# Kernel tuning notes

Measured on AMD Instinct MI355X. Metric: run time of the kernel, lower is better.

Reference implementation:

```python
import jax, jax.numpy as jnp
import numpy as np

N_NODES = 100000
N_EDGES = 1600000
IN_CH = 128
OUT_CH = 64
HID = 2 * OUT_CH  # 128


def _gcn_conv(x, src, dst, deg_inv_sqrt, W, b, n_nodes):
    """PyG GCNConv with symmetric normalization; self-loops already in (src, dst)."""
    h = x @ W                                   # [N, F_out] dense GEMM
    norm = deg_inv_sqrt[src] * deg_inv_sqrt[dst]  # [E+N]
    msg = h[src] * norm[:, None]                # gather + scale (irregular)
    out = jax.ops.segment_sum(msg, dst, num_segments=n_nodes)  # scatter-add
    return out + b


def setup_inputs() -> dict:
    key = jax.random.key(0)
    ks = jax.random.split(key, 8)
    x = jax.random.normal(ks[0], (N_NODES, IN_CH), dtype=jnp.float32)
    edge_index = jax.random.randint(ks[1], (2, N_EDGES), 0, N_NODES, dtype=jnp.int64)
    # Glorot-ish params for the three GCNConv layers
    W1 = jax.random.normal(ks[2], (IN_CH, HID), dtype=jnp.float32) / np.sqrt(IN_CH)
    b1 = jnp.zeros((HID,), dtype=jnp.float32)
    W_mu = jax.random.normal(ks[3], (HID, OUT_CH), dtype=jnp.float32) / np.sqrt(HID)
    b_mu = jnp.zeros((OUT_CH,), dtype=jnp.float32)
    W_ls = jax.random.normal(ks[4], (HID, OUT_CH), dtype=jnp.float32) / np.sqrt(HID)
    b_ls = jnp.zeros((OUT_CH,), dtype=jnp.float32)
    return {"x": x, "edge_index": edge_index, "W1": W1, "b1": b1,
            "W_mu": W_mu, "b_mu": b_mu, "W_ls": W_ls, "b_ls": b_ls}


def reference(x, edge_index, W1, b1, W_mu, b_mu, W_ls, b_ls):
    n = x.shape[0]
    # GCNConv adds self-loops to the same edge_index in every layer; do it once.
    loop = jnp.arange(n, dtype=edge_index.dtype)
    src = jnp.concatenate([edge_index[0], loop])  # source / row
    dst = jnp.concatenate([edge_index[1], loop])  # target / col
    # Symmetric normalization: deg over targets with unit edge weights.
    deg = jax.ops.segment_sum(jnp.ones_like(dst, dtype=x.dtype), dst, num_segments=n)
    deg_inv_sqrt = jnp.where(deg > 0, jax.lax.rsqrt(jnp.maximum(deg, 1.0)), 0.0)

    h = jax.nn.relu(_gcn_conv(x, src, dst, deg_inv_sqrt, W1, b1, n))
    mu = _gcn_conv(h, src, dst, deg_inv_sqrt, W_mu, b_mu, n)
    logstd = _gcn_conv(h, src, dst, deg_inv_sqrt, W_ls, b_ls, n)
    return mu, logstd
```

## Files before the change

### kernel.cpp

```cpp
#include <hip/hip_runtime.h>
#include <hip/hip_bf16.h>
#include <stdint.h>


static inline size_t align_up(size_t x, size_t a) { return (x + a - 1) / a * a; }

typedef __attribute__((ext_vector_type(8))) short short8;
typedef __attribute__((ext_vector_type(4))) float f32x4;

#define BSHIFT 7
#define BNODES 128
#define CHUNKS 512
#define NBMAX 1024

__device__ inline unsigned short f2bf(float f) {
    unsigned u = __float_as_uint(f);
    unsigned r = (u + 0x7FFFu + ((u >> 16) & 1u)) >> 16;
    return (unsigned short)r;
}
__device__ inline float bf2f(unsigned v16) {
    return __uint_as_float(v16 << 16);
}


__global__ void detect_i64_kernel(const int* __restrict__ ei, int nwords_check, int* __restrict__ flag) {
    __shared__ int any_nz;
    if (threadIdx.x == 0) any_nz = 0;
    __syncthreads();
    int nz = 0;
    for (int i = threadIdx.x; i < nwords_check; i += blockDim.x) {
        if (ei[2 * i + 1] != 0) nz = 1;
    }
    if (nz) atomicOr(&any_nz, 1);
    __syncthreads();
    if (threadIdx.x == 0) flag[0] = any_nz ? 0 : 1;
}

__device__ inline int load_idx(const void* ei, const int* flag, size_t pos, int n) {
    int v;
    if (flag[0]) v = (int)((const long long*)ei)[pos];
    else         v = ((const int*)ei)[pos];
    return (v < 0) ? 0 : (v >= n ? n - 1 : v);
}


__global__ __launch_bounds__(256) void chunk_hist_kernel(
        const void* __restrict__ ei, const int* __restrict__ flag,
        int* __restrict__ hmat, int E, int n, int nb, int epc) {
    __shared__ int hist[NBMAX];
    const int c = blockIdx.x, t = threadIdx.x;
    for (int i = t; i < nb; i += 256) hist[i] = 0;
    __syncthreads();
    const int lo = c * epc, hi = min(E, lo + epc);
    for (int i = lo + t; i < hi; i += 256) {
        int d = load_idx(ei, flag, (size_t)E + i, n);
        atomicAdd(&hist[d >> BSHIFT], 1);
    }
    __syncthreads();
    for (int i = t; i < nb; i += 256) hmat[(size_t)c * nb + i] = hist[i];
}


__global__ __launch_bounds__(256) void bucket_scan_cols_kernel(
        int* __restrict__ hmat, int* __restrict__ btot, int nb) {
    __shared__ int tmp[256];
    const int b = blockIdx.x, t = threadIdx.x;
    const int c0 = 2 * t;
    int va = hmat[(size_t)c0 * nb + b];
    int vb = hmat[(size_t)(c0 + 1) * nb + b];
    int pair = va + vb;
    tmp[t] = pair;
    __syncthreads();
    for (int off = 1; off < 256; off <<= 1) {
        int u = (t >= off) ? tmp[t - off] : 0;
        __syncthreads();
        tmp[t] += u;
        __syncthreads();
    }
    int excl = tmp[t] - pair;
    hmat[(size_t)c0 * nb + b] = excl;
    hmat[(size_t)(c0 + 1) * nb + b] = excl + va;
    if (t == 255) btot[b] = tmp[255];
}


__global__ void base_scan_kernel(const int* __restrict__ btot, int* __restrict__ bbase, int nb) {
    __shared__ int tmp[NBMAX];
    int t = threadIdx.x;
    int v = (t < nb) ? btot[t] : 0;
    tmp[t] = v;
    __syncthreads();
    for (int off = 1; off < NBMAX; off <<= 1) {
        int u = (t >= off) ? tmp[t - off] : 0;
        __syncthreads();
        tmp[t] += u;
        __syncthreads();
    }
    if (t < nb) bbase[t] = tmp[t] - v;
}


__global__ __launch_bounds__(256) void chunk_scatter_kernel(
        const void* __restrict__ ei, const int* __restrict__ flag,
        const int* __restrict__ hmat, const int* __restrict__ bbase,
        unsigned* __restrict__ binned, int E, int n, int nb, int epc) {
    __shared__ int lcur[NBMAX];
    const int c = blockIdx.x, t = threadIdx.x;
    for (int i = t; i < nb; i += 256) lcur[i] = hmat[(size_t)c * nb + i] + bbase[i];
    __syncthreads();
    const int lo = c * epc, hi = min(E, lo + epc);
    for (int i = lo + t; i < hi; i += 256) {
        int s = load_idx(ei, flag, i, n);
        int d = load_idx(ei, flag, (size_t)E + i, n);
        int b = d >> BSHIFT;
        int pos = atomicAdd(&lcur[b], 1);
        binned[pos] = ((unsigned)s << BSHIFT) | (unsigned)(d & (BNODES - 1));
    }
}


__global__ __launch_bounds__(256) void bucket_csr_kernel(
        const unsigned* __restrict__ binned, const int* __restrict__ bbase,
        const int* __restrict__ btot, float* __restrict__ dis,
        int* __restrict__ row_beg, int* __restrict__ row_end,
        int* __restrict__ csr_src, int n) {
    __shared__ int ldeg[BNODES];
    __shared__ int lscan[BNODES];
    __shared__ int lcur[BNODES];
    const int b = blockIdx.x;
    const int t = threadIdx.x;
    const int base = bbase[b];
    const int cnt = btot[b];

    if (t < BNODES) ldeg[t] = 0;
    __syncthreads();
    for (int i = t; i < cnt; i += 256) {
        unsigned w = binned[base + i];
        atomicAdd(&ldeg[w & (BNODES - 1)], 1);
    }
    __syncthreads();
    int v = (t < BNODES) ? ldeg[t] : 0;
    if (t < BNODES) lscan[t] = v;
    __syncthreads();
    for (int off = 1; off < BNODES; off <<= 1) {
        int u = (t < BNODES && t >= off) ? lscan[t - off] : 0;
        __syncthreads();
        if (t < BNODES) lscan[t] += u;
        __syncthreads();
    }
    if (t < BNODES) {
        int excl = lscan[t] - v;
        lcur[t] = excl;
        int node = (b << BSHIFT) + t;
        if (node < n) {
            dis[node] = rsqrtf((float)v + 1.0f);
            row_beg[node] = base + excl;
            row_end[node] = base + excl + v;
        }
    }
    __syncthreads();
    for (int i = t; i < cnt; i += 256) {
        unsigned w = binned[base + i];
        int pos = atomicAdd(&lcur[w & (BNODES - 1)], 1);
        csr_src[base + pos] = (int)(w >> BSHIFT);
    }
}


__global__ void prep_weights_kernel(const float* __restrict__ W1,
                                    const float* __restrict__ Wmu,
                                    const float* __restrict__ Wls,
                                    unsigned short* __restrict__ Wt1,
                                    unsigned short* __restrict__ Wtcat) {
    int idx = blockIdx.x * 256 + threadIdx.x;
    if (idx < 16384) {
        int c = idx >> 7, k = idx & 127;
        Wt1[c * 128 + k] = f2bf(W1[k * 128 + c]);
    } else if (idx < 32768) {
        int i = idx - 16384;
        int j = i >> 7, k = i & 127;
        float v = (j < 64) ? Wmu[k * 64 + j] : Wls[k * 64 + (j - 64)];
        Wtcat[j * 128 + k] = f2bf(v);
    }
}


template <int MODE>
__global__ __launch_bounds__(256) void mfma_gemm_kernel(
        const void* __restrict__ Ax, const unsigned short* __restrict__ Wt,
        const float* __restrict__ biasA, const float* __restrict__ biasB,
        void* __restrict__ outA, void* __restrict__ outB, int n) {
    __shared__ unsigned short ws[128 * 136];
    const int tid = threadIdx.x;
    const int wave = tid >> 6, lane = tid & 63;
    const int brow = blockIdx.x * 64 + wave * 16;
    const int lr = lane & 15;
    const int kg = lane >> 4;
    const int k0 = kg * 8;

    for (int i = tid; i < 2048; i += 256) {
        int r = i >> 4, ci = i & 15;
        *(short8*)&ws[r * 136 + ci * 8] = *(const short8*)&Wt[r * 128 + ci * 8];
    }
    __syncthreads();

    int arow = brow + lr;
    if (arow >= n) arow = n - 1;

    f32x4 acc[8];
#pragma unroll
    for (int t = 0; t < 8; ++t) acc[t] = (f32x4){0.f, 0.f, 0.f, 0.f};

#pragma unroll
    for (int c = 0; c < 4; ++c) {
        short8 a;
        if (MODE == 0) {
            const float* ap = (const float*)Ax + (size_t)arow * 128 + c * 32 + k0;
            float4 lo = *(const float4*)ap;
            float4 hi = *(const float4*)(ap + 4);
            a[0] = (short)f2bf(lo.x); a[1] = (short)f2bf(lo.y);
            a[2] = (short)f2bf(lo.z); a[3] = (short)f2bf(lo.w);
            a[4] = (short)f2bf(hi.x); a[5] = (short)f2bf(hi.y);
            a[6] = (short)f2bf(hi.z); a[7] = (short)f2bf(hi.w);
        } else {
            a = *(const short8*)((const unsigned short*)Ax + (size_t)arow * 128 + c * 32 + k0);
        }
#pragma unroll
        for (int t = 0; t < 8; ++t) {
            short8 bfr = *(const short8*)&ws[(t * 16 + lr) * 136 + c * 32 + k0];
            acc[t] = __builtin_amdgcn_mfma_f32_16x16x32_bf16(a, bfr, acc[t], 0, 0, 0);
        }
    }

    if (MODE == 0) {
        unsigned short* out = (unsigned short*)outA;
#pragma unroll
        for (int t = 0; t < 8; ++t) {
            int col = t * 16 + lr;
#pragma unroll
            for (int r = 0; r < 4; ++r) {
                int row = brow + kg * 4 + r;
                if (row < n) out[(size_t)row * 128 + col] = f2bf(acc[t][r]);
            }
        }
    } else {
        float* oA = (float*)outA;
        float* oB = (float*)outB;
#pragma unroll
        for (int t = 0; t < 8; ++t) {
            int col = t * 16 + lr;
            float bv = (col < 64) ? biasA[col] : biasB[col - 64];
#pragma unroll
            for (int r = 0; r < 4; ++r) {
                int row = brow + kg * 4 + r;
                if (row < n) {
                    float v = acc[t][r] + bv;
                    if (col < 64) oA[(size_t)row * 64 + col] = v;
                    else          oB[(size_t)row * 64 + (col - 64)] = v;
                }
            }
        }
    }
}


__global__ __launch_bounds__(256) void csr_agg_kernel(
        const unsigned short* __restrict__ hin, const int* __restrict__ row_beg,
        const int* __restrict__ row_end, const int* __restrict__ csr_src,
        const float* __restrict__ dis, const float* __restrict__ bias,
        unsigned short* __restrict__ out, int n, int relu) {
    int node = blockIdx.x * 4 + (threadIdx.x >> 6);
    if (node >= n) return;
    const int lane = threadIdx.x & 63;
    const int hi_half = lane >> 5;
    const unsigned foff = (lane & 31) * 8;
    int beg = row_beg[node], end = row_end[node];
    float dv = dis[node];

    const char* hinb = (const char*)hin;

    float a0x = 0.f, a0y = 0.f, a0z = 0.f, a0w = 0.f;
    float a1x = 0.f, a1y = 0.f, a1z = 0.f, a1w = 0.f;
    float a2x = 0.f, a2y = 0.f, a2z = 0.f, a2w = 0.f;
    float a3x = 0.f, a3y = 0.f, a3z = 0.f, a3w = 0.f;

    int e = beg;
    for (; e + 7 < end; e += 8) {
        int s0 = csr_src[e + 0 + hi_half];
        int s1 = csr_src[e + 2 + hi_half];
        int s2 = csr_src[e + 4 + hi_half];
        int s3 = csr_src[e + 6 + hi_half];
        float w0 = dis[s0], w1 = dis[s1], w2 = dis[s2], w3 = dis[s3];
        uint2 d0 = *(const uint2*)(hinb + (size_t)s0 * 256 + foff);
        uint2 d1 = *(const uint2*)(hinb + (size_t)s1 * 256 + foff);
        uint2 d2 = *(const uint2*)(hinb + (size_t)s2 * 256 + foff);
        uint2 d3 = *(const uint2*)(hinb + (size_t)s3 * 256 + foff);
        a0x += bf2f(d0.x & 0xffffu) * w0; a0y += bf2f(d0.x >> 16) * w0;
        a0z += bf2f(d0.y & 0xffffu) * w0; a0w += bf2f(d0.y >> 16) * w0;
        a1x += bf2f(d1.x & 0xffffu) * w1; a1y += bf2f(d1.x >> 16) * w1;
        a1z += bf2f(d1.y & 0xffffu) * w1; a1w += bf2f(d1.y >> 16) * w1;
        a2x += bf2f(d2.x & 0xffffu) * w2; a2y += bf2f(d2.x >> 16) * w2;
        a2z += bf2f(d2.y & 0xffffu) * w2; a2w += bf2f(d2.y >> 16) * w2;
        a3x += bf2f(d3.x & 0xffffu) * w3; a3y += bf2f(d3.x >> 16) * w3;
        a3z += bf2f(d3.y & 0xffffu) * w3; a3w += bf2f(d3.y >> 16) * w3;
    }
    for (; e + 1 < end; e += 2) {
        int s = csr_src[e + hi_half];
        float w = dis[s];
        uint2 d = *(const uint2*)(hinb + (size_t)s * 256 + foff);
        a0x += bf2f(d.x & 0xffffu) * w; a0y += bf2f(d.x >> 16) * w;
        a0z += bf2f(d.y & 0xffffu) * w; a0w += bf2f(d.y >> 16) * w;
    }
    if (e < end) {
        int s = csr_src[e];
        float w = 0.5f * dis[s];
        uint2 d = *(const uint2*)(hinb + (size_t)s * 256 + foff);
        a1x += bf2f(d.x & 0xffffu) * w; a1y += bf2f(d.x >> 16) * w;
        a1z += bf2f(d.y & 0xffffu) * w; a1w += bf2f(d.y >> 16) * w;
    }

    float sx = (a0x + a1x) + (a2x + a3x);
    float sy = (a0y + a1y) + (a2y + a3y);
    float sz = (a0z + a1z) + (a2z + a3z);
    float sw = (a0w + a1w) + (a2w + a3w);
    sx += __shfl_xor(sx, 32, 64);
    sy += __shfl_xor(sy, 32, 64);
    sz += __shfl_xor(sz, 32, 64);
    sw += __shfl_xor(sw, 32, 64);

    uint2 sd = *(const uint2*)(hinb + (size_t)node * 256 + foff);
    sx = dv * (sx + dv * bf2f(sd.x & 0xffffu));
    sy = dv * (sy + dv * bf2f(sd.x >> 16));
    sz = dv * (sz + dv * bf2f(sd.y & 0xffffu));
    sw = dv * (sw + dv * bf2f(sd.y >> 16));

    if (bias) {
        float4 bb = *(const float4*)&bias[(lane & 31) * 4];
        sx += bb.x; sy += bb.y; sz += bb.z; sw += bb.w;
    }
    if (relu) {
        sx = fmaxf(sx, 0.f); sy = fmaxf(sy, 0.f);
        sz = fmaxf(sz, 0.f); sw = fmaxf(sw, 0.f);
    }
    if (lane < 32) {
        uint2 o;
        o.x = (unsigned)f2bf(sx) | ((unsigned)f2bf(sy) << 16);
        o.y = (unsigned)f2bf(sz) | ((unsigned)f2bf(sw) << 16);
        *(uint2*)((char*)out + (size_t)node * 256 + foff) = o;
    }
}


extern "C" void kernel_launch(void* const* d_in, const int* in_sizes, int n_in,
                              void* d_out, int out_size, void* d_ws, size_t ws_size,
                              hipStream_t stream) {
    const float* x   = (const float*)d_in[0];
    const void*  ei  = d_in[1];
    const float* W1  = (const float*)d_in[2];
    const float* b1  = (const float*)d_in[3];
    const float* Wmu = (const float*)d_in[4];
    const float* bmu = (const float*)d_in[5];
    const float* Wls = (const float*)d_in[6];
    const float* bls = (const float*)d_in[7];

    const int n = in_sizes[0] / 128;
    const int E = in_sizes[1] / 2;
    const int nb = (n + BNODES - 1) >> BSHIFT;
    const int epc = (E + CHUNKS - 1) / CHUNKS;

    float* out   = (float*)d_out;
    float* outMu = out;
    float* outLs = out + (size_t)n * 64;

    char* w = (char*)d_ws;
    auto alloc = [&](size_t bytes) { char* p = w; w += align_up(bytes, 256); return p; };
    int*            flag    = (int*)           alloc(256);
    int*            hmat    = (int*)           alloc((size_t)CHUNKS * nb * 4);
    int*            btot    = (int*)           alloc(NBMAX * 4);
    int*            bbase   = (int*)           alloc(NBMAX * 4);
    unsigned*       binned  = (unsigned*)      alloc((size_t)E * 4);
    int*            row_beg = (int*)           alloc((size_t)n * 4);
    int*            row_end = (int*)           alloc((size_t)n * 4);
    float*          dis     = (float*)         alloc((size_t)n * 4);
    int*            csr_src = (int*)           alloc((size_t)E * 4);
    unsigned short* Wt1     = (unsigned short*)alloc(128 * 128 * 2);
    unsigned short* Wtcat   = (unsigned short*)alloc(128 * 128 * 2);
    unsigned short* xW      = (unsigned short*)alloc((size_t)n * 128 * 2);
    unsigned short* h       = (unsigned short*)alloc((size_t)n * 128 * 2);
    unsigned short* hagg    = (unsigned short*)alloc((size_t)n * 128 * 2);

    detect_i64_kernel<<<1, 256, 0, stream>>>((const int*)ei, 1024, flag);
    chunk_hist_kernel<<<CHUNKS, 256, 0, stream>>>(ei, flag, hmat, E, n, nb, epc);
    bucket_scan_cols_kernel<<<nb, 256, 0, stream>>>(hmat, btot, nb);
    base_scan_kernel<<<1, NBMAX, 0, stream>>>(btot, bbase, nb);
    chunk_scatter_kernel<<<CHUNKS, 256, 0, stream>>>(ei, flag, hmat, bbase, binned, E, n, nb, epc);
    bucket_csr_kernel<<<nb, 256, 0, stream>>>(binned, bbase, btot, dis, row_beg, row_end,
                                              csr_src, n);
    prep_weights_kernel<<<128, 256, 0, stream>>>(W1, Wmu, Wls, Wt1, Wtcat);

    const int gblocks = (n + 63) / 64;

    mfma_gemm_kernel<0><<<gblocks, 256, 0, stream>>>(x, Wt1, nullptr, nullptr, xW, nullptr, n);
    csr_agg_kernel<<<(n + 3) / 4, 256, 0, stream>>>(xW, row_beg, row_end, csr_src,
                                                    dis, b1, h, n, 1);

    csr_agg_kernel<<<(n + 3) / 4, 256, 0, stream>>>(h, row_beg, row_end, csr_src,
                                                    dis, nullptr, hagg, n, 0);
    mfma_gemm_kernel<1><<<gblocks, 256, 0, stream>>>(hagg, Wtcat, bmu, bls, outMu, outLs, n);
}
```

Baseline: 239.5 us.

## Fuse second aggregation with output GEMM and inline int64 index detection

Merges the layer-2 CSR aggregation and the mu/logstd GEMM into one kernel. Each 1024-thread block aggregates 16 nodes into shared memory and then runs MFMA against the concatenated weights, which removes the hagg round trip through global memory. It also drops the separate int64-detection kernel by having each chunk block probe its own range. The trade-off is that every 16-node block reloads the full 128x128 weight tile into LDS, and half the waves sit idle during the GEMM phase.

```diff
diff --git a/kernel.cpp b/kernel.cpp
--- a/kernel.cpp
+++ b/kernel.cpp
@@ -22,38 +22,40 @@
     return __uint_as_float(v16 << 16);
 }
 
-
-__global__ void detect_i64_kernel(const int* __restrict__ ei, int nwords_check, int* __restrict__ flag) {
-    __shared__ int any_nz;
-    if (threadIdx.x == 0) any_nz = 0;
+__device__ inline bool detect_i64_local(const void* ei, int lo, int hi, int t) {
+    __shared__ int s_nz;
+    if (t == 0) s_nz = 0;
     __syncthreads();
     int nz = 0;
-    for (int i = threadIdx.x; i < nwords_check; i += blockDim.x) {
-        if (ei[2 * i + 1] != 0) nz = 1;
-    }
-    if (nz) atomicOr(&any_nz, 1);
-    __syncthreads();
-    if (threadIdx.x == 0) flag[0] = any_nz ? 0 : 1;
-}
-
-__device__ inline int load_idx(const void* ei, const int* flag, size_t pos, int n) {
+    int lim = min(hi, lo + 1024);
+    const int* p = (const int*)ei;
+    for (int i = lo + t; i < lim; i += 256) {
+        if (p[2 * i + 1] != 0) nz = 1;
+    }
+    if (nz) atomicOr(&s_nz, 1);
+    __syncthreads();
+    return s_nz == 0;
+}
+
+__device__ inline int load_idx2(const void* ei, bool is64, size_t pos, int n) {
     int v;
-    if (flag[0]) v = (int)((const long long*)ei)[pos];
-    else         v = ((const int*)ei)[pos];
+    if (is64) v = (int)((const long long*)ei)[pos];
+    else      v = ((const int*)ei)[pos];
     return (v < 0) ? 0 : (v >= n ? n - 1 : v);
 }
 
 
 __global__ __launch_bounds__(256) void chunk_hist_kernel(
-        const void* __restrict__ ei, const int* __restrict__ flag,
-        int* __restrict__ hmat, int E, int n, int nb, int epc) {
+        const void* __restrict__ ei, int* __restrict__ hmat,
+        int E, int n, int nb, int epc) {
     __shared__ int hist[NBMAX];
     const int c = blockIdx.x, t = threadIdx.x;
+    const int lo = min(E, c * epc), hi = min(E, lo + epc);
+    bool is64 = detect_i64_local(ei, lo, hi, t);
     for (int i = t; i < nb; i += 256) hist[i] = 0;
     __syncthreads();
-    const int lo = c * epc, hi = min(E, lo + epc);
     for (int i = lo + t; i < hi; i += 256) {
-        int d = load_idx(ei, flag, (size_t)E + i, n);
+        int d = load_idx2(ei, is64, (size_t)E + i, n);
         atomicAdd(&hist[d >> BSHIFT], 1);
     }
     __syncthreads();
@@ -101,17 +103,18 @@
 
 
 __global__ __launch_bounds__(256) void chunk_scatter_kernel(
-        const void* __restrict__ ei, const int* __restrict__ flag,
-        const int* __restrict__ hmat, const int* __restrict__ bbase,
-        unsigned* __restrict__ binned, int E, int n, int nb, int epc) {
+        const void* __restrict__ ei, const int* __restrict__ hmat,
+        const int* __restrict__ bbase, unsigned* __restrict__ binned,
+        int E, int n, int nb, int epc) {
     __shared__ int lcur[NBMAX];
     const int c = blockIdx.x, t = threadIdx.x;
+    const int lo = min(E, c * epc), hi = min(E, lo + epc);
+    bool is64 = detect_i64_local(ei, lo, hi, t);
     for (int i = t; i < nb; i += 256) lcur[i] = hmat[(size_t)c * nb + i] + bbase[i];
     __syncthreads();
-    const int lo = c * epc, hi = min(E, lo + epc);
     for (int i = lo + t; i < hi; i += 256) {
-        int s = load_idx(ei, flag, i, n);
-        int d = load_idx(ei, flag, (size_t)E + i, n);
+        int s = load_idx2(ei, is64, i, n);
+        int d = load_idx2(ei, is64, (size_t)E + i, n);
         int b = d >> BSHIFT;
         int pos = atomicAdd(&lcur[b], 1);
         binned[pos] = ((unsigned)s << BSHIFT) | (unsigned)(d & (BNODES - 1));
@@ -185,11 +188,9 @@
 }
 
 
-template <int MODE>
 __global__ __launch_bounds__(256) void mfma_gemm_kernel(
-        const void* __restrict__ Ax, const unsigned short* __restrict__ Wt,
-        const float* __restrict__ biasA, const float* __restrict__ biasB,
-        void* __restrict__ outA, void* __restrict__ outB, int n) {
+        const float* __restrict__ Ax, const unsigned short* __restrict__ Wt,
+        unsigned short* __restrict__ outB16, int n) {
     __shared__ unsigned short ws[128 * 136];
     const int tid = threadIdx.x;
     const int wave = tid >> 6, lane = tid & 63;
@@ -213,18 +214,14 @@
 
 #pragma unroll
     for (int c = 0; c < 4; ++c) {
+        const float* ap = Ax + (size_t)arow * 128 + c * 32 + k0;
+        float4 lo = *(const float4*)ap;
+        float4 hi = *(const float4*)(ap + 4);
         short8 a;
-        if (MODE == 0) {
-            const float* ap = (const float*)Ax + (size_t)arow * 128 + c * 32 + k0;
-            float4 lo = *(const float4*)ap;
-            float4 hi = *(const float4*)(ap + 4);
-            a[0] = (short)f2bf(lo.x); a[1] = (short)f2bf(lo.y);
-            a[2] = (short)f2bf(lo.z); a[3] = (short)f2bf(lo.w);
-            a[4] = (short)f2bf(hi.x); a[5] = (short)f2bf(hi.y);
-            a[6] = (short)f2bf(hi.z); a[7] = (short)f2bf(hi.w);
-        } else {
-            a = *(const short8*)((const unsigned short*)Ax + (size_t)arow * 128 + c * 32 + k0);
-        }
+        a[0] = (short)f2bf(lo.x); a[1] = (short)f2bf(lo.y);
+        a[2] = (short)f2bf(lo.z); a[3] = (short)f2bf(lo.w);
+        a[4] = (short)f2bf(hi.x); a[5] = (short)f2bf(hi.y);
+        a[6] = (short)f2bf(hi.z); a[7] = (short)f2bf(hi.w);
 #pragma unroll
         for (int t = 0; t < 8; ++t) {
             short8 bfr = *(const short8*)&ws[(t * 16 + lr) * 136 + c * 32 + k0];
@@ -232,52 +229,26 @@
         }
     }
 
-    if (MODE == 0) {
-        unsigned short* out = (unsigned short*)outA;
-#pragma unroll
-        for (int t = 0; t < 8; ++t) {
-            int col = t * 16 + lr;
-#pragma unroll
-            for (int r = 0; r < 4; ++r) {
-                int row = brow + kg * 4 + r;
-                if (row < n) out[(size_t)row * 128 + col] = f2bf(acc[t][r]);
-            }
-        }
-    } else {
-        float* oA = (float*)outA;
-        float* oB = (float*)outB;
-#pragma unroll
-        for (int t = 0; t < 8; ++t) {
-            int col = t * 16 + lr;
-            float bv = (col < 64) ? biasA[col] : biasB[col - 64];
-#pragma unroll
-            for (int r = 0; r < 4; ++r) {
-                int row = brow + kg * 4 + r;
-                if (row < n) {
-                    float v = acc[t][r] + bv;
-                    if (col < 64) oA[(size_t)row * 64 + col] = v;
-                    else          oB[(size_t)row * 64 + (col - 64)] = v;
-                }
-            }
-        }
-    }
-}
-
-
-__global__ __launch_bounds__(256) void csr_agg_kernel(
-        const unsigned short* __restrict__ hin, const int* __restrict__ row_beg,
+#pragma unroll
+    for (int t = 0; t < 8; ++t) {
+        int col = t * 16 + lr;
+#pragma unroll
+        for (int r = 0; r < 4; ++r) {
+            int row = brow + kg * 4 + r;
+            if (row < n) outB16[(size_t)row * 128 + col] = f2bf(acc[t][r]);
+        }
+    }
+}
+
+
+__device__ inline float4 agg_node(
+        const char* __restrict__ hinb, const int* __restrict__ row_beg,
         const int* __restrict__ row_end, const int* __restrict__ csr_src,
-        const float* __restrict__ dis, const float* __restrict__ bias,
-        unsigned short* __restrict__ out, int n, int relu) {
-    int node = blockIdx.x * 4 + (threadIdx.x >> 6);
-    if (node >= n) return;
-    const int lane = threadIdx.x & 63;
+        const float* __restrict__ dis, int node, int lane) {
     const int hi_half = lane >> 5;
     const unsigned foff = (lane & 31) * 8;
     int beg = row_beg[node], end = row_end[node];
     float dv = dis[node];
-
-    const char* hinb = (const char*)hin;
 
     float a0x = 0.f, a0y = 0.f, a0z = 0.f, a0w = 0.f;
     float a1x = 0.f, a1y = 0.f, a1z = 0.f, a1w = 0.f;
@@ -329,24 +300,92 @@
     sw += __shfl_xor(sw, 32, 64);
 
     uint2 sd = *(const uint2*)(hinb + (size_t)node * 256 + foff);
-    sx = dv * (sx + dv * bf2f(sd.x & 0xffffu));
-    sy = dv * (sy + dv * bf2f(sd.x >> 16));
-    sz = dv * (sz + dv * bf2f(sd.y & 0xffffu));
-    sw = dv * (sw + dv * bf2f(sd.y >> 16));
-
-    if (bias) {
+    float4 r;
+    r.x = dv * (sx + dv * bf2f(sd.x & 0xffffu));
+    r.y = dv * (sy + dv * bf2f(sd.x >> 16));
+    r.z = dv * (sz + dv * bf2f(sd.y & 0xffffu));
+    r.w = dv * (sw + dv * bf2f(sd.y >> 16));
+    return r;
+}
+
+
+__global__ __launch_bounds__(256) void csr_agg_kernel(
+        const unsigned short* __restrict__ hin, const int* __restrict__ row_beg,
+        const int* __restrict__ row_end, const int* __restrict__ csr_src,
+        const float* __restrict__ dis, const float* __restrict__ bias,
+        unsigned short* __restrict__ out, int n) {
+    int node = blockIdx.x * 4 + (threadIdx.x >> 6);
+    if (node >= n) return;
+    const int lane = threadIdx.x & 63;
+    float4 s = agg_node((const char*)hin, row_beg, row_end, csr_src, dis, node, lane);
+    if (lane < 32) {
         float4 bb = *(const float4*)&bias[(lane & 31) * 4];
-        sx += bb.x; sy += bb.y; sz += bb.z; sw += bb.w;
-    }
-    if (relu) {
-        sx = fmaxf(sx, 0.f); sy = fmaxf(sy, 0.f);
-        sz = fmaxf(sz, 0.f); sw = fmaxf(sw, 0.f);
-    }
-    if (lane < 32) {
+        s.x = fmaxf(s.x + bb.x, 0.f);
+        s.y = fmaxf(s.y + bb.y, 0.f);
+        s.z = fmaxf(s.z + bb.z, 0.f);
+        s.w = fmaxf(s.w + bb.w, 0.f);
         uint2 o;
-        o.x = (unsigned)f2bf(sx) | ((unsigned)f2bf(sy) << 16);
-        o.y = (unsigned)f2bf(sz) | ((unsigned)f2bf(sw) << 16);
-        *(uint2*)((char*)out + (size_t)node * 256 + foff) = o;
+        o.x = (unsigned)f2bf(s.x) | ((unsigned)f2bf(s.y) << 16);
+        o.y = (unsigned)f2bf(s.z) | ((unsigned)f2bf(s.w) << 16);
+        *(uint2*)((char*)out + (size_t)node * 256 + (lane & 31) * 8) = o;
+    }
+}
+
+
+__global__ __launch_bounds__(1024) void agg2_gemm_fused_kernel(
+        const unsigned short* __restrict__ hin, const int* __restrict__ row_beg,
+        const int* __restrict__ row_end, const int* __restrict__ csr_src,
+        const float* __restrict__ dis, const unsigned short* __restrict__ Wt,
+        const float* __restrict__ biasA, const float* __restrict__ biasB,
+        float* __restrict__ outA, float* __restrict__ outB, int n) {
+    __shared__ unsigned short hs[16 * 136];
+    __shared__ unsigned short ws[128 * 136];
+    const int tid = threadIdx.x;
+    const int wave = tid >> 6, lane = tid & 63;
+    const int node0 = blockIdx.x * 16;
+    const int node = node0 + wave;
+
+    for (int i = tid; i < 2048; i += 1024) {
+        int r = i >> 4, ci = i & 15;
+        *(short8*)&ws[r * 136 + ci * 8] = *(const short8*)&Wt[r * 128 + ci * 8];
+    }
+
+    if (node < n) {
+        float4 s = agg_node((const char*)hin, row_beg, row_end, csr_src, dis, node, lane);
+        if (lane < 32) {
+            uint2 o;
+            o.x = (unsigned)f2bf(s.x) | ((unsigned)f2bf(s.y) << 16);
+            o.y = (unsigned)f2bf(s.z) | ((unsigned)f2bf(s.w) << 16);
+            *(uint2*)((char*)hs + wave * 272 + (lane & 31) * 8) = o;
+        }
+    } else if (lane < 32) {
+        uint2 z = make_uint2(0u, 0u);
+        *(uint2*)((char*)hs + wave * 272 + (lane & 31) * 8) = z;
+    }
+    __syncthreads();
+
+    if (wave < 8) {
+        const int lr = lane & 15;
+        const int kg = lane >> 4;
+        const int k0 = kg * 8;
+        f32x4 acc = (f32x4){0.f, 0.f, 0.f, 0.f};
+#pragma unroll
+        for (int c = 0; c < 4; ++c) {
+            short8 a = *(const short8*)&hs[lr * 136 + c * 32 + k0];
+            short8 b = *(const short8*)&ws[(wave * 16 + lr) * 136 + c * 32 + k0];
+            acc = __builtin_amdgcn_mfma_f32_16x16x32_bf16(a, b, acc, 0, 0, 0);
+        }
+        int col = wave * 16 + lr;
+        float bv = (col < 64) ? biasA[col] : biasB[col - 64];
+#pragma unroll
+        for (int r = 0; r < 4; ++r) {
+            int row = node0 + kg * 4 + r;
+            if (row < n) {
+                float v = acc[r] + bv;
+                if (col < 64) outA[(size_t)row * 64 + col] = v;
+                else          outB[(size_t)row * 64 + (col - 64)] = v;
+            }
+        }
     }
 }
 
@@ -374,7 +413,6 @@
 
     char* w = (char*)d_ws;
     auto alloc = [&](size_t bytes) { char* p = w; w += align_up(bytes, 256); return p; };
-    int*            flag    = (int*)           alloc(256);
     int*            hmat    = (int*)           alloc((size_t)CHUNKS * nb * 4);
     int*            btot    = (int*)           alloc(NBMAX * 4);
     int*            bbase   = (int*)           alloc(NBMAX * 4);
@@ -387,24 +425,21 @@
     unsigned short* Wtcat   = (unsigned short*)alloc(128 * 128 * 2);
     unsigned short* xW      = (unsigned short*)alloc((size_t)n * 128 * 2);
     unsigned short* h       = (unsigned short*)alloc((size_t)n * 128 * 2);
-    unsigned short* hagg    = (unsigned short*)alloc((size_t)n * 128 * 2);
-
-    detect_i64_kernel<<<1, 256, 0, stream>>>((const int*)ei, 1024, flag);
-    chunk_hist_kernel<<<CHUNKS, 256, 0, stream>>>(ei, flag, hmat, E, n, nb, epc);
+
+    chunk_hist_kernel<<<CHUNKS, 256, 0, stream>>>(ei, hmat, E, n, nb, epc);
     bucket_scan_cols_kernel<<<nb, 256, 0, stream>>>(hmat, btot, nb);
     base_scan_kernel<<<1, NBMAX, 0, stream>>>(btot, bbase, nb);
-    chunk_scatter_kernel<<<CHUNKS, 256, 0, stream>>>(ei, flag, hmat, bbase, binned, E, n, nb, epc);
+    chunk_scatter_kernel<<<CHUNKS, 256, 0, stream>>>(ei, hmat, bbase, binned, E, n, nb, epc);
     bucket_csr_kernel<<<nb, 256, 0, stream>>>(binned, bbase, btot, dis, row_beg, row_end,
                                               csr_src, n);
     prep_weights_kernel<<<128, 256, 0, stream>>>(W1, Wmu, Wls, Wt1, Wtcat);
 
     const int gblocks = (n + 63) / 64;
 
-    mfma_gemm_kernel<0><<<gblocks, 256, 0, stream>>>(x, Wt1, nullptr, nullptr, xW, nullptr, n);
+    mfma_gemm_kernel<<<gblocks, 256, 0, stream>>>(x, Wt1, xW, n);
     csr_agg_kernel<<<(n + 3) / 4, 256, 0, stream>>>(xW, row_beg, row_end, csr_src,
-                                                    dis, b1, h, n, 1);
-
-    csr_agg_kernel<<<(n + 3) / 4, 256, 0, stream>>>(h, row_beg, row_end, csr_src,
-                                                    dis, nullptr, hagg, n, 0);
-    mfma_gemm_kernel<1><<<gblocks, 256, 0, stream>>>(hagg, Wtcat, bmu, bls, outMu, outLs, n);
-}
+                                                    dis, b1, h, n);
+
+    agg2_gemm_fused_kernel<<<(n + 15) / 16, 1024, 0, stream>>>(
+        h, row_beg, row_end, csr_src, dis, Wtcat, bmu, bls, outMu, outLs, n);
+}
```

Measured after the change: 245.7 us. 1.03x slower.

## Process aggregation nodes in descending-degree order via counting-sort permutation

Applied to the files above, without the earlier changes.

Builds a node permutation sorted by in-degree (descending) with a chunked counting sort, and has both CSR aggregation kernels walk nodes through that permutation so heavy rows start first and waves within a block get similar work. It also removes the separate int64-detection launch by having each edge-processing block check its own chunk. The cost is four extra small kernel launches plus an indirection through perm, which scatters output rows and may hurt write locality. With uniform random edges the degree spread is narrow, so the balancing benefit may be small.

```diff
diff --git a/kernel.cpp b/kernel.cpp
--- a/kernel.cpp
+++ b/kernel.cpp
@@ -12,6 +12,8 @@
 #define BNODES 128
 #define CHUNKS 512
 #define NBMAX 1024
+#define NCHUNKN 256
+#define DBINS 256
 
 __device__ inline unsigned short f2bf(float f) {
     unsigned u = __float_as_uint(f);
@@ -22,38 +24,40 @@
     return __uint_as_float(v16 << 16);
 }
 
-
-__global__ void detect_i64_kernel(const int* __restrict__ ei, int nwords_check, int* __restrict__ flag) {
-    __shared__ int any_nz;
-    if (threadIdx.x == 0) any_nz = 0;
+__device__ inline bool detect_i64_local(const void* ei, int lo, int hi, int t) {
+    __shared__ int s_nz;
+    if (t == 0) s_nz = 0;
     __syncthreads();
     int nz = 0;
-    for (int i = threadIdx.x; i < nwords_check; i += blockDim.x) {
-        if (ei[2 * i + 1] != 0) nz = 1;
-    }
-    if (nz) atomicOr(&any_nz, 1);
-    __syncthreads();
-    if (threadIdx.x == 0) flag[0] = any_nz ? 0 : 1;
-}
-
-__device__ inline int load_idx(const void* ei, const int* flag, size_t pos, int n) {
+    int lim = min(hi, lo + 1024);
+    const int* p = (const int*)ei;
+    for (int i = lo + t; i < lim; i += 256) {
+        if (p[2 * i + 1] != 0) nz = 1;
+    }
+    if (nz) atomicOr(&s_nz, 1);
+    __syncthreads();
+    return s_nz == 0;
+}
+
+__device__ inline int load_idx2(const void* ei, bool is64, size_t pos, int n) {
     int v;
-    if (flag[0]) v = (int)((const long long*)ei)[pos];
-    else         v = ((const int*)ei)[pos];
+    if (is64) v = (int)((const long long*)ei)[pos];
+    else      v = ((const int*)ei)[pos];
     return (v < 0) ? 0 : (v >= n ? n - 1 : v);
 }
 
 
 __global__ __launch_bounds__(256) void chunk_hist_kernel(
-        const void* __restrict__ ei, const int* __restrict__ flag,
-        int* __restrict__ hmat, int E, int n, int nb, int epc) {
+        const void* __restrict__ ei, int* __restrict__ hmat,
+        int E, int n, int nb, int epc) {
     __shared__ int hist[NBMAX];
     const int c = blockIdx.x, t = threadIdx.x;
+    const int lo = min(E, c * epc), hi = min(E, lo + epc);
+    bool is64 = detect_i64_local(ei, lo, hi, t);
     for (int i = t; i < nb; i += 256) hist[i] = 0;
     __syncthreads();
-    const int lo = c * epc, hi = min(E, lo + epc);
     for (int i = lo + t; i < hi; i += 256) {
-        int d = load_idx(ei, flag, (size_t)E + i, n);
+        int d = load_idx2(ei, is64, (size_t)E + i, n);
         atomicAdd(&hist[d >> BSHIFT], 1);
     }
     __syncthreads();
@@ -101,17 +105,18 @@
 
 
 __global__ __launch_bounds__(256) void chunk_scatter_kernel(
-        const void* __restrict__ ei, const int* __restrict__ flag,
-        const int* __restrict__ hmat, const int* __restrict__ bbase,
-        unsigned* __restrict__ binned, int E, int n, int nb, int epc) {
+        const void* __restrict__ ei, const int* __restrict__ hmat,
+        const int* __restrict__ bbase, unsigned* __restrict__ binned,
+        int E, int n, int nb, int epc) {
     __shared__ int lcur[NBMAX];
     const int c = blockIdx.x, t = threadIdx.x;
+    const int lo = min(E, c * epc), hi = min(E, lo + epc);
+    bool is64 = detect_i64_local(ei, lo, hi, t);
     for (int i = t; i < nb; i += 256) lcur[i] = hmat[(size_t)c * nb + i] + bbase[i];
     __syncthreads();
-    const int lo = c * epc, hi = min(E, lo + epc);
     for (int i = lo + t; i < hi; i += 256) {
-        int s = load_idx(ei, flag, i, n);
-        int d = load_idx(ei, flag, (size_t)E + i, n);
+        int s = load_idx2(ei, is64, i, n);
+        int d = load_idx2(ei, is64, (size_t)E + i, n);
         int b = d >> BSHIFT;
         int pos = atomicAdd(&lcur[b], 1);
         binned[pos] = ((unsigned)s << BSHIFT) | (unsigned)(d & (BNODES - 1));
@@ -163,6 +168,56 @@
         unsigned w = binned[base + i];
         int pos = atomicAdd(&lcur[w & (BNODES - 1)], 1);
         csr_src[base + pos] = (int)(w >> BSHIFT);
+    }
+}
+
+
+__global__ __launch_bounds__(256) void node_deg_hist_kernel(
+        const int* __restrict__ row_beg, const int* __restrict__ row_end,
+        int* __restrict__ dh, int n, int npc) {
+    __shared__ int hist[DBINS];
+    const int c = blockIdx.x, t = threadIdx.x;
+    hist[t] = 0;
+    __syncthreads();
+    const int lo = min(n, c * npc), hi = min(n, lo + npc);
+    for (int i = lo + t; i < hi; i += 256) {
+        int bin = (DBINS - 1) - min(row_end[i] - row_beg[i], DBINS - 1);
+        atomicAdd(&hist[bin], 1);
+    }
+    __syncthreads();
+    dh[c * DBINS + t] = hist[t];
+}
+
+__global__ __launch_bounds__(256) void deg_scan_cols_kernel(
+        int* __restrict__ dh, int* __restrict__ dtot) {
+    __shared__ int tmp[NCHUNKN];
+    const int b = blockIdx.x, t = threadIdx.x;
+    int v = dh[t * DBINS + b];
+    tmp[t] = v;
+    __syncthreads();
+    for (int off = 1; off < NCHUNKN; off <<= 1) {
+        int u = (t >= off) ? tmp[t - off] : 0;
+        __syncthreads();
+        tmp[t] += u;
+        __syncthreads();
+    }
+    dh[t * DBINS + b] = tmp[t] - v;
+    if (t == NCHUNKN - 1) dtot[b] = tmp[NCHUNKN - 1];
+}
+
+__global__ __launch_bounds__(256) void node_perm_scatter_kernel(
+        const int* __restrict__ row_beg, const int* __restrict__ row_end,
+        const int* __restrict__ dh, const int* __restrict__ dbase,
+        int* __restrict__ perm, int n, int npc) {
+    __shared__ int cur[DBINS];
+    const int c = blockIdx.x, t = threadIdx.x;
+    cur[t] = dh[c * DBINS + t] + dbase[t];
+    __syncthreads();
+    const int lo = min(n, c * npc), hi = min(n, lo + npc);
+    for (int i = lo + t; i < hi; i += 256) {
+        int bin = (DBINS - 1) - min(row_end[i] - row_beg[i], DBINS - 1);
+        int pos = atomicAdd(&cur[bin], 1);
+        perm[pos] = i;
     }
 }
 
@@ -267,10 +322,12 @@
 __global__ __launch_bounds__(256) void csr_agg_kernel(
         const unsigned short* __restrict__ hin, const int* __restrict__ row_beg,
         const int* __restrict__ row_end, const int* __restrict__ csr_src,
-        const float* __restrict__ dis, const float* __restrict__ bias,
-        unsigned short* __restrict__ out, int n, int relu) {
-    int node = blockIdx.x * 4 + (threadIdx.x >> 6);
-    if (node >= n) return;
+        const int* __restrict__ perm, const float* __restrict__ dis,
+        const float* __restrict__ bias, unsigned short* __restrict__ out,
+        int n, int relu) {
+    int gid = blockIdx.x * 4 + (threadIdx.x >> 6);
+    if (gid >= n) return;
+    int node = perm[gid];
     const int lane = threadIdx.x & 63;
     const int hi_half = lane >> 5;
     const unsigned foff = (lane & 31) * 8;
@@ -367,6 +424,7 @@
     const int E = in_sizes[1] / 2;
     const int nb = (n + BNODES - 1) >> BSHIFT;
     const int epc = (E + CHUNKS - 1) / CHUNKS;
+    const int npc = (n + NCHUNKN - 1) / NCHUNKN;
 
     float* out   = (float*)d_out;
     float* outMu = out;
@@ -374,7 +432,6 @@
 
     char* w = (char*)d_ws;
     auto alloc = [&](size_t bytes) { char* p = w; w += align_up(bytes, 256); return p; };
-    int*            flag    = (int*)           alloc(256);
     int*            hmat    = (int*)           alloc((size_t)CHUNKS * nb * 4);
     int*            btot    = (int*)           alloc(NBMAX * 4);
     int*            bbase   = (int*)           alloc(NBMAX * 4);
@@ -383,28 +440,38 @@
     int*            row_end = (int*)           alloc((size_t)n * 4);
     float*          dis     = (float*)         alloc((size_t)n * 4);
     int*            csr_src = (int*)           alloc((size_t)E * 4);
+    int*            dh      = (int*)           alloc((size_t)NCHUNKN * DBINS * 4);
+    int*            dtot    = (int*)           alloc(DBINS * 4);
+    int*            dbase   = (int*)           alloc(DBINS * 4);
+    int*            perm    = (int*)           alloc((size_t)n * 4);
     unsigned short* Wt1     = (unsigned short*)alloc(128 * 128 * 2);
     unsigned short* Wtcat   = (unsigned short*)alloc(128 * 128 * 2);
     unsigned short* xW      = (unsigned short*)alloc((size_t)n * 128 * 2);
     unsigned short* h       = (unsigned short*)alloc((size_t)n * 128 * 2);
     unsigned short* hagg    = (unsigned short*)alloc((size_t)n * 128 * 2);
 
-    detect_i64_kernel<<<1, 256, 0, stream>>>((const int*)ei, 1024, flag);
-    chunk_hist_kernel<<<CHUNKS, 256, 0, stream>>>(ei, flag, hmat, E, n, nb, epc);
+    chunk_hist_kernel<<<CHUNKS, 256, 0, stream>>>(ei, hmat, E, n, nb, epc);
     bucket_scan_cols_kernel<<<nb, 256, 0, stream>>>(hmat, btot, nb);
     base_scan_kernel<<<1, NBMAX, 0, stream>>>(btot, bbase, nb);
-    chunk_scatter_kernel<<<CHUNKS, 256, 0, stream>>>(ei, flag, hmat, bbase, binned, E, n, nb, epc);
+    chunk_scatter_kernel<<<CHUNKS, 256, 0, stream>>>(ei, hmat, bbase, binned, E, n, nb, epc);
     bucket_csr_kernel<<<nb, 256, 0, stream>>>(binned, bbase, btot, dis, row_beg, row_end,
                                               csr_src, n);
+
+    node_deg_hist_kernel<<<NCHUNKN, 256, 0, stream>>>(row_beg, row_end, dh, n, npc);
+    deg_scan_cols_kernel<<<DBINS, NCHUNKN, 0, stream>>>(dh, dtot);
+    base_scan_kernel<<<1, NBMAX, 0, stream>>>(dtot, dbase, DBINS);
+    node_perm_scatter_kernel<<<NCHUNKN, 256, 0, stream>>>(row_beg, row_end, dh, dbase,
+                                                          perm, n, npc);
+
     prep_weights_kernel<<<128, 256, 0, stream>>>(W1, Wmu, Wls, Wt1, Wtcat);
 
     const int gblocks = (n + 63) / 64;
 
     mfma_gemm_kernel<0><<<gblocks, 256, 0, stream>>>(x, Wt1, nullptr, nullptr, xW, nullptr, n);
-    csr_agg_kernel<<<(n + 3) / 4, 256, 0, stream>>>(xW, row_beg, row_end, csr_src,
+    csr_agg_kernel<<<(n + 3) / 4, 256, 0, stream>>>(xW, row_beg, row_end, csr_src, perm,
                                                     dis, b1, h, n, 1);
 
-    csr_agg_kernel<<<(n + 3) / 4, 256, 0, stream>>>(h, row_beg, row_end, csr_src,
+    csr_agg_kernel<<<(n + 3) / 4, 256, 0, stream>>>(h, row_beg, row_end, csr_src, perm,
                                                     dis, nullptr, hagg, n, 0);
     mfma_gemm_kernel<1><<<gblocks, 256, 0, stream>>>(hagg, Wtcat, bmu, bls, outMu, outLs, n);
 }
```

After: 253.7 us. 5.9% more time.
